# Kernel optimization log

Measured on AMD Instinct MI355X. Metric: run time of the kernel, lower is better.

## Reference

```python
import jax, jax.numpy as jnp
import numpy as np
import math

DIM = 1024
NUM_HEADS = 16
HEAD_DIM = DIM // NUM_HEADS


def build_rope_matrix(dim, seq_len):
    # (seq_len, dim): concat of cos(freqs) and sin(freqs), each (seq_len, dim//2)
    position = jnp.arange(seq_len, dtype=jnp.float32)[:, None]
    dim_pair = jnp.arange(0, dim, 2, dtype=jnp.float32)[None, :]
    theta = 10000.0 ** (-dim_pair / dim)
    freqs = position * theta  # (seq_len, dim//2)
    return jnp.concatenate([jnp.cos(freqs), jnp.sin(freqs)], axis=-1)


def apply_rope(x, rope):
    # x: (..., N, d), rope: (N, d). Faithful to the torch code's strided slicing.
    x1, x2 = x[..., ::2], x[..., 1::2]
    cos = rope[..., ::2]
    sin = rope[..., 1::2]
    return jnp.concatenate([x1 * cos - x2 * sin, x1 * sin + x2 * cos], axis=-1)


def setup_inputs() -> dict:
    key = jax.random.key(0)
    ks = jax.random.split(key, 9)
    B, N = 2, 2048
    x = jax.random.normal(ks[0], (B, N, DIM), dtype=jnp.float32)
    # Xavier-uniform-ish linear weights (dim, dim), zero-mean biases
    bound = math.sqrt(6.0 / (DIM + DIM))
    def w(k):
        return jax.random.uniform(k, (DIM, DIM), jnp.float32, -bound, bound)
    def b(k):
        return jax.random.uniform(k, (DIM,), jnp.float32, -1.0 / math.sqrt(DIM), 1.0 / math.sqrt(DIM))
    return {
        "x": x,
        "Wq": w(ks[1]), "bq": b(ks[2]),
        "Wk": w(ks[3]), "bk": b(ks[4]),
        "Wv": w(ks[5]), "bv": b(ks[6]),
        "Wo": w(ks[7]), "bo": b(ks[8]),
    }


def reference(x, Wq, bq, Wk, bk, Wv, bv, Wo, bo):
    B, N, _ = x.shape
    H, hd = NUM_HEADS, HEAD_DIM
    rope = build_rope_matrix(hd, N)  # (N, hd)

    def proj(W, bias):
        y = x @ W.T + bias               # (B, N, dim)
        return y.reshape(B, N, H, hd).transpose(0, 2, 1, 3)  # (B, H, N, hd)

    q = apply_rope(proj(Wq, bq), rope)
    k = apply_rope(proj(Wk, bk), rope)
    v = apply_rope(proj(Wv, bv), rope)

    scores = jnp.einsum("bhqd,bhkd->bhqk", q, k) / math.sqrt(hd)
    probs = jax.nn.softmax(scores, axis=-1)
    out = jnp.einsum("bhqk,bhkd->bhqd", probs, v)  # (B, H, N, hd)

    out = apply_rope(out, -rope)  # inverse RoPE (as defined: negate rope)
    out = out.transpose(0, 2, 1, 3).reshape(B, N, DIM)
    return out @ Wo.T + bo
```

## Files before the change

### kernel.cpp

```cpp
#include <hip/hip_runtime.h>
#include <hip/hip_bf16.h>
#include <math.h>

#define NHEADS 16
#define HDIM   64
#define BATCH  2
#define SEQLEN 2048
#define DIMSZ  1024

typedef _Float16 f16x8 __attribute__((ext_vector_type(8)));
typedef _Float16 f16x4 __attribute__((ext_vector_type(4)));
typedef float    f32x4 __attribute__((ext_vector_type(4)));
typedef unsigned short u16x8 __attribute__((ext_vector_type(8)));
typedef unsigned int   u32x4 __attribute__((ext_vector_type(4)));

__device__ __forceinline__ float rope_theta(int c) {
    int i = c & 31;
    return (float)pow(10000.0, -(double)i / 32.0);
}
__device__ __forceinline__ unsigned short f16u(float f) {
    _Float16 h = (_Float16)f;
    return *reinterpret_cast<unsigned short*>(&h);
}
__device__ __forceinline__ void async_copy16(const void* gsrc, void* lds) {
    __builtin_amdgcn_global_load_lds(
        (const __attribute__((address_space(1))) unsigned int*)gsrc,
        (__attribute__((address_space(3))) unsigned int*)lds, 16, 0, 0);
}

__global__ __launch_bounds__(256) void prep_kernel(
    const float* __restrict__ x, const float* __restrict__ Wq,
    const float* __restrict__ Wk, const float* __restrict__ Wv,
    const float* __restrict__ Wo, const float* __restrict__ bq,
    const float* __restrict__ bk, const float* __restrict__ bv,
    unsigned short* __restrict__ x16, unsigned short* __restrict__ Wqkv16,
    unsigned short* __restrict__ Wo16, float* __restrict__ biasqkv,
    float* __restrict__ ropeC, float* __restrict__ ropeS)
{
    const int NV = (4194304 + 4 * 1048576) / 8;
    int gid = blockIdx.x * 256 + threadIdx.x;
    for (int i = gid; i < NV; i += gridDim.x * 256) {
        long e = (long)i * 8;
        const float* src; unsigned short* dst; long off;
        if (e < 4194304)      { src = x;  dst = x16;              off = e; }
        else if (e < 5242880) { src = Wq; dst = Wqkv16;           off = e - 4194304; }
        else if (e < 6291456) { src = Wk; dst = Wqkv16 + 1048576; off = e - 5242880; }
        else if (e < 7340032) { src = Wv; dst = Wqkv16 + 2097152; off = e - 6291456; }
        else                  { src = Wo; dst = Wo16;             off = e - 7340032; }
        float4 v0 = *reinterpret_cast<const float4*>(src + off);
        float4 v1 = *reinterpret_cast<const float4*>(src + off + 4);
        u16x8 o;
        o[0] = f16u(v0.x); o[1] = f16u(v0.y); o[2] = f16u(v0.z); o[3] = f16u(v0.w);
        o[4] = f16u(v1.x); o[5] = f16u(v1.y); o[6] = f16u(v1.z); o[7] = f16u(v1.w);
        *reinterpret_cast<u16x8*>(dst + off) = o;
    }
    if (gid < 65536) {
        int npos = gid >> 5, j = gid & 31;
        float f = (float)npos * rope_theta(j);
        ropeC[gid] = cosf(f);
        ropeS[gid] = sinf(f);
    }
    if (gid < 3072) {
        biasqkv[gid] = gid < 1024 ? bq[gid] : (gid < 2048 ? bk[gid - 1024] : bv[gid - 2048]);
    }
}

__global__ __launch_bounds__(512, 4) void qkv_gemm_kernel(
    const unsigned short* __restrict__ A, const unsigned short* __restrict__ B,
    const float* __restrict__ bias, const float* __restrict__ ropeC,
    const float* __restrict__ ropeS, unsigned short* __restrict__ QKV)
{
    __shared__ __align__(16) unsigned char smem[65536];
    const int tid = threadIdx.x;
    const int w = tid >> 6, l = tid & 63;
    const int g = l >> 4, lx = l & 15;
    const int wr = w >> 2, wc = w & 3;
    const int row0 = blockIdx.y * 128;
    const int col0 = blockIdx.x * 128;
    const unsigned short* Ab = A + (size_t)row0 * DIMSZ;
    const unsigned short* Bb = B + (size_t)col0 * DIMSZ;

    const int sr = tid >> 3;
    const int sc = tid & 7;
    const int ssw = sc ^ (sr & 7);
    const size_t sAoff0 = (size_t)sr * DIMSZ + ssw * 8;
    const size_t sAoff1 = (size_t)(64 + sr) * DIMSZ + ssw * 8;

    f32x4 acc[4][2] = {};
    async_copy16(Ab + sAoff0, smem + tid * 16);
    async_copy16(Ab + sAoff1, smem + 8192 + tid * 16);
    async_copy16(Bb + sAoff0, smem + 16384 + tid * 16);
    async_copy16(Bb + sAoff1, smem + 16384 + 8192 + tid * 16);
    __syncthreads();

    int buf = 0;
    for (int k0 = 0; k0 < DIMSZ; k0 += 64) {
        if (k0 + 64 < DIMSZ) {
            const int nb = (buf ^ 1) * 32768;
            async_copy16(Ab + sAoff0 + k0 + 64, smem + nb + tid * 16);
            async_copy16(Ab + sAoff1 + k0 + 64, smem + nb + 8192 + tid * 16);
            async_copy16(Bb + sAoff0 + k0 + 64, smem + nb + 16384 + tid * 16);
            async_copy16(Bb + sAoff1 + k0 + 64, smem + nb + 16384 + 8192 + tid * 16);
        }
        const int ab = buf * 32768, bb2 = ab + 16384;
        #pragma unroll
        for (int ks = 0; ks < 2; ++ks) {
            f16x8 af[4], bf[2];
            #pragma unroll
            for (int m = 0; m < 4; ++m) {
                int r = wr * 64 + m * 16 + lx;
                af[m] = *reinterpret_cast<const f16x8*>(
                    &smem[ab + r * 128 + ((ks * 64 + g * 16) ^ ((r & 7) << 4))]);
            }
            #pragma unroll
            for (int n = 0; n < 2; ++n) {
                int r = wc * 32 + n * 16 + lx;
                bf[n] = *reinterpret_cast<const f16x8*>(
                    &smem[bb2 + r * 128 + ((ks * 64 + g * 16) ^ ((r & 7) << 4))]);
            }
            #pragma unroll
            for (int m = 0; m < 4; ++m)
                #pragma unroll
                for (int n = 0; n < 2; ++n)
                    acc[m][n] = __builtin_amdgcn_mfma_f32_16x16x32_f16(af[m], bf[n], acc[m][n], 0, 0, 0);
        }
        __syncthreads();
        buf ^= 1;
    }

    const int proj = col0 >> 10;
    const int cin128 = (col0 & 1023);
    float bsv[2];
    #pragma unroll
    for (int n = 0; n < 2; ++n) bsv[n] = bias[col0 + wc * 32 + n * 16 + lx];

    if (proj == 2) {
        _Float16* T = (_Float16*)smem;
        #pragma unroll
        for (int m = 0; m < 4; ++m) {
            int rl0 = wr * 64 + m * 16 + g * 4;
            #pragma unroll
            for (int r2 = 0; r2 < 4; ++r2) {
                int rlocal = rl0 + r2;
                int npos = (row0 + rlocal) & (SEQLEN - 1);
                const float* rcp = ropeC + npos * 32;
                const float* rsp = ropeS + npos * 32;
                #pragma unroll
                for (int n = 0; n < 2; ++n) {
                    float v = acc[m][n][r2] + bsv[n];
                    float o = __shfl_xor(v, 1);
                    int dcol = wc * 32 + n * 16 + lx;
                    int c = dcol & 63;
                    const float* tab = (c < 32) ? rcp : rsp;
                    float Rd = tab[c & 31];
                    float Rp = tab[(c & 31) ^ 1];
                    float y; int outc;
                    if (c & 1) { y = o * Rd + v * Rp; outc = (c >> 1) + 32; }
                    else       { y = v * Rd - o * Rp; outc = c >> 1; }
                    T[((dcol >> 6) * 64 + outc) * 136 + rlocal] = (_Float16)y;
                }
            }
        }
        __syncthreads();
        int b = row0 >> 11, npos0 = row0 & (SEQLEN - 1);
        int hd0 = cin128 >> 6;
        int trow = tid >> 2;
        int cbase = (tid & 3) * 32;
        int head = hd0 + (trow >> 6);
        int outd = trow & 63;
        unsigned short* vdst = QKV + 8388608 +
            (((size_t)b * NHEADS + head) * HDIM + outd) * SEQLEN + npos0 + cbase;
        #pragma unroll
        for (int i2 = 0; i2 < 4; ++i2) {
            f16x8 val = *reinterpret_cast<const f16x8*>(&T[trow * 136 + cbase + i2 * 8]);
            *reinterpret_cast<f16x8*>(vdst + i2 * 8) = val;
        }
    } else {
        #pragma unroll
        for (int m = 0; m < 4; ++m) {
            int rbase = row0 + wr * 64 + m * 16 + g * 4;
            #pragma unroll
            for (int r2 = 0; r2 < 4; ++r2) {
                int rglob = rbase + r2;
                int b = rglob >> 11, npos = rglob & (SEQLEN - 1);
                const float* rcp = ropeC + npos * 32;
                const float* rsp = ropeS + npos * 32;
                #pragma unroll
                for (int n = 0; n < 2; ++n) {
                    float v = acc[m][n][r2] + bsv[n];
                    float o = __shfl_xor(v, 1);
                    int hd = (cin128 + wc * 32 + n * 16) >> 6;
                    int c = ((wc * 32 + n * 16) & 63) + lx;
                    const float* tab = (c < 32) ? rcp : rsp;
                    float Rd = tab[c & 31];
                    float Rp = tab[(c & 31) ^ 1];
                    float y; int outc;
                    if (c & 1) { y = o * Rd + v * Rp; outc = (c >> 1) + 32; }
                    else       { y = v * Rd - o * Rp; outc = c >> 1; }
                    unsigned short* Orow = QKV +
                        ((((size_t)proj * BATCH + b) * NHEADS + hd) * SEQLEN + npos) * HDIM;
                    Orow[outc] = f16u(y);
                }
            }
        }
    }
}

__global__ __launch_bounds__(512, 8) void attn_mfma_kernel(
    const unsigned short* __restrict__ QKV, const float* __restrict__ ropeC,
    const float* __restrict__ ropeS, unsigned short* __restrict__ Y)
{
    __shared__ __align__(16) unsigned char smem[32768];
    const int tid = threadIdx.x;
    const int w   = tid >> 6;
    const int l   = tid & 63;
    const int g   = l >> 4;
    const int lx  = l & 15;
    const int qg  = w & 3;
    const int kh  = w >> 2;
    const int fb  = blockIdx.x;
    const int xcd = fb & 7, jj = fb >> 3;
    const int bh  = xcd * 4 + (jj & 3);
    const int b   = bh >> 4;
    const int h   = bh & 15;
    const int q0  = (jj >> 2) * 64;

    const unsigned short* Qb  = QKV + (size_t)bh * SEQLEN * HDIM;
    const unsigned short* Kb  = QKV + 4194304 + (size_t)bh * SEQLEN * HDIM;
    const unsigned short* Vtb = QKV + 8388608 + (size_t)bh * SEQLEN * HDIM;

    f16x8 qf[2];
    {
        const unsigned short* src = Qb + (size_t)(q0 + qg * 16 + lx) * HDIM + g * 8;
        qf[0] = *reinterpret_cast<const f16x8*>(src);
        qf[1] = *reinterpret_cast<const f16x8*>(src + 32);
    }
    f16x8 ones8;
    #pragma unroll
    for (int i = 0; i < 8; ++i) ones8[i] = (_Float16)1.0f;

    const float K2 = 0.18033688011112043f;
    f32x4 oacc[4] = {};
    f32x4 lsum = {};
    float mrow = -1e30f;

    const int srow = tid >> 3;
    const int c8   = tid & 7;
    const int sch  = c8 ^ (srow & 7);
    const int sdst = tid * 16;
    const int kperm = (srow & 32) + (((srow >> 2) & 3) << 3) + (((srow >> 4) & 1) << 2) + (srow & 3);

    async_copy16(Kb  + (size_t)kperm * HDIM + sch * 8, smem + sdst);
    async_copy16(Vtb + (size_t)srow * SEQLEN + sch * 8, smem + 8192 + sdst);
    __syncthreads();

    int buf = 0;
    for (int kt = 0; kt < SEQLEN / 64; ++kt) {
        if (kt + 1 < SEQLEN / 64) {
            const int k0n = (kt + 1) * 64;
            const int nb = (buf ^ 1) * 16384;
            async_copy16(Kb  + (size_t)(k0n + kperm) * HDIM + sch * 8,
                         smem + nb + sdst);
            async_copy16(Vtb + (size_t)srow * SEQLEN + k0n + sch * 8,
                         smem + nb + 8192 + sdst);
        }
        const int kb = buf * 16384;
        const int vb = kb + 8192;

        f32x4 sacc[2] = {};
        __builtin_amdgcn_s_setprio(1);
        #pragma unroll
        for (int c = 0; c < 2; ++c) {
            int row = kh * 32 + c * 16 + lx;
            int rowb = kb + row * 128, sw = (row & 7) << 4;
            f16x8 k0f = *reinterpret_cast<const f16x8*>(&smem[rowb + ((g * 16) ^ sw)]);
            f16x8 k1f = *reinterpret_cast<const f16x8*>(&smem[rowb + ((64 + g * 16) ^ sw)]);
            sacc[c] = __builtin_amdgcn_mfma_f32_16x16x32_f16(k0f, qf[0], sacc[c], 0, 0, 0);
            sacc[c] = __builtin_amdgcn_mfma_f32_16x16x32_f16(k1f, qf[1], sacc[c], 0, 0, 0);
        }
        __builtin_amdgcn_s_setprio(0);

        float lmax = sacc[0][0];
        #pragma unroll
        for (int c = 0; c < 2; ++c)
            #pragma unroll
            for (int r = 0; r < 4; ++r) lmax = fmaxf(lmax, sacc[c][r]);
        bool ok = (lmax <= mrow + 64.f);
        if (!__all((int)ok)) {
            float m2 = fmaxf(lmax, __shfl_xor(lmax, 16));
            m2 = fmaxf(m2, __shfl_xor(m2, 32));
            float mnew = fmaxf(mrow, m2);
            float sc = exp2f((mrow - mnew) * K2);
            mrow = mnew;
            #pragma unroll
            for (int r = 0; r < 4; ++r) lsum[r] *= sc;
            #pragma unroll
            for (int c = 0; c < 4; ++c)
                #pragma unroll
                for (int r = 0; r < 4; ++r) oacc[c][r] *= sc;
        }
        float mk = -mrow * K2;
        #pragma unroll
        for (int c = 0; c < 2; ++c)
            #pragma unroll
            for (int r = 0; r < 4; ++r)
                sacc[c][r] = exp2f(fmaf(sacc[c][r], K2, mk));

        u32x4 pw;
        pw[0] = __builtin_bit_cast(unsigned, __builtin_amdgcn_cvt_pkrtz(sacc[0][0], sacc[0][1]));
        pw[1] = __builtin_bit_cast(unsigned, __builtin_amdgcn_cvt_pkrtz(sacc[0][2], sacc[0][3]));
        pw[2] = __builtin_bit_cast(unsigned, __builtin_amdgcn_cvt_pkrtz(sacc[1][0], sacc[1][1]));
        pw[3] = __builtin_bit_cast(unsigned, __builtin_amdgcn_cvt_pkrtz(sacc[1][2], sacc[1][3]));
        f16x8 pfrag = __builtin_bit_cast(f16x8, pw);

        __builtin_amdgcn_s_setprio(1);
        lsum = __builtin_amdgcn_mfma_f32_16x16x32_f16(ones8, pfrag, lsum, 0, 0, 0);
        #pragma unroll
        for (int c2 = 0; c2 < 4; ++c2) {
            int d = c2 * 16 + lx;
            f16x8 vf8 = *reinterpret_cast<const f16x8*>(
                &smem[vb + d * 128 + ((kh * 64 + g * 16) ^ ((d & 7) << 4))]);
            oacc[c2] = __builtin_amdgcn_mfma_f32_16x16x32_f16(vf8, pfrag, oacc[c2], 0, 0, 0);
        }
        __builtin_amdgcn_s_setprio(0);

        __syncthreads();
        buf ^= 1;
    }

    float* Of = (float*)smem + qg * 1120;
    if (kh == 1) {
        #pragma unroll
        for (int c2 = 0; c2 < 4; ++c2)
            *reinterpret_cast<f32x4*>(&Of[lx * 68 + c2 * 16 + g * 4]) = oacc[c2];
        if (g == 0) {
            Of[1088 + lx] = mrow;
            Of[1104 + lx] = lsum[0];
        }
    }
    __syncthreads();
    if (kh == 0) {
        float m_hi = Of[1088 + lx];
        float l_hi = Of[1104 + lx];
        float M = fmaxf(mrow, m_hi);
        float a  = exp2f((mrow - M) * K2);
        float bb = exp2f((m_hi - M) * K2);
        float inv = 1.0f / (a * lsum[0] + bb * l_hi);
        const int q = q0 + qg * 16 + lx;
        unsigned short* drow = Y + ((size_t)b * SEQLEN + q) * DIMSZ + h * HDIM;
        #pragma unroll
        for (int c2 = 0; c2 < 4; ++c2) {
            f32x4 ohi = *reinterpret_cast<const f32x4*>(&Of[lx * 68 + c2 * 16 + g * 4]);
            const float* tab = ((c2 < 2) ? ropeC : ropeS) + (size_t)q * 32;
            unsigned short lo16[2], hi16[2];
            #pragma unroll
            for (int rp = 0; rp < 2; ++rp) {
                int d = c2 * 16 + g * 4 + 2 * rp;
                float v0 = (a * oacc[c2][2 * rp]     + bb * ohi[2 * rp])     * inv;
                float v1 = (a * oacc[c2][2 * rp + 1] + bb * ohi[2 * rp + 1]) * inv;
                float Rd = tab[d & 31], Rn = tab[(d & 31) + 1];
                lo16[rp] = f16u(-(v0 * Rd - v1 * Rn));
                hi16[rp] = f16u(-(v0 * Rn + v1 * Rd));
            }
            int p = c2 * 8 + g * 2;
            *reinterpret_cast<unsigned*>(&drow[p])      = (unsigned)lo16[0] | ((unsigned)lo16[1] << 16);
            *reinterpret_cast<unsigned*>(&drow[p + 32]) = (unsigned)hi16[0] | ((unsigned)hi16[1] << 16);
        }
    }
}

__global__ __launch_bounds__(512, 4) void out_gemm_kernel(
    const unsigned short* __restrict__ A, const unsigned short* __restrict__ B,
    const float* __restrict__ bias, float* __restrict__ Out)
{
    __shared__ __align__(16) unsigned char smem[65536];
    const int tid = threadIdx.x;
    const int w = tid >> 6, l = tid & 63;
    const int g = l >> 4, lx = l & 15;
    const int wr = w >> 2, wc = w & 3;
    const int row0 = blockIdx.y * 128;
    const int col0 = blockIdx.x * 128;
    const unsigned short* Ab = A + (size_t)row0 * DIMSZ;
    const unsigned short* Bb = B + (size_t)col0 * DIMSZ;

    const int sr = tid >> 3;
    const int sc = tid & 7;
    const int ssw = sc ^ (sr & 7);
    const size_t sAoff0 = (size_t)sr * DIMSZ + ssw * 8;
    const size_t sAoff1 = (size_t)(64 + sr) * DIMSZ + ssw * 8;

    f32x4 acc[4][2] = {};
    async_copy16(Ab + sAoff0, smem + tid * 16);
    async_copy16(Ab + sAoff1, smem + 8192 + tid * 16);
    async_copy16(Bb + sAoff0, smem + 16384 + tid * 16);
    async_copy16(Bb + sAoff1, smem + 16384 + 8192 + tid * 16);
    __syncthreads();

    int buf = 0;
    for (int k0 = 0; k0 < DIMSZ; k0 += 64) {
        if (k0 + 64 < DIMSZ) {
            const int nb = (buf ^ 1) * 32768;
            async_copy16(Ab + sAoff0 + k0 + 64, smem + nb + tid * 16);
            async_copy16(Ab + sAoff1 + k0 + 64, smem + nb + 8192 + tid * 16);
            async_copy16(Bb + sAoff0 + k0 + 64, smem + nb + 16384 + tid * 16);
            async_copy16(Bb + sAoff1 + k0 + 64, smem + nb + 16384 + 8192 + tid * 16);
        }
        const int ab = buf * 32768, bb2 = ab + 16384;
        #pragma unroll
        for (int ks = 0; ks < 2; ++ks) {
            f16x8 af[4], bf[2];
            #pragma unroll
            for (int m = 0; m < 4; ++m) {
                int r = wr * 64 + m * 16 + lx;
                af[m] = *reinterpret_cast<const f16x8*>(
                    &smem[ab + r * 128 + ((ks * 64 + g * 16) ^ ((r & 7) << 4))]);
            }
            #pragma unroll
            for (int n = 0; n < 2; ++n) {
                int r = wc * 32 + n * 16 + lx;
                bf[n] = *reinterpret_cast<const f16x8*>(
                    &smem[bb2 + r * 128 + ((ks * 64 + g * 16) ^ ((r & 7) << 4))]);
            }
            #pragma unroll
            for (int m = 0; m < 4; ++m)
                #pragma unroll
                for (int n = 0; n < 2; ++n)
                    acc[m][n] = __builtin_amdgcn_mfma_f32_16x16x32_f16(af[m], bf[n], acc[m][n], 0, 0, 0);
        }
        __syncthreads();
        buf ^= 1;
    }

    const int cb0 = col0 + wc * 32;
    float bsv[2];
    #pragma unroll
    for (int n = 0; n < 2; ++n) bsv[n] = bias[cb0 + n * 16 + lx];
    #pragma unroll
    for (int m = 0; m < 4; ++m) {
        int rbase = row0 + wr * 64 + m * 16 + g * 4;
        #pragma unroll
        for (int r2 = 0; r2 < 4; ++r2) {
            float* orow = Out + (size_t)(rbase + r2) * DIMSZ + cb0;
            #pragma unroll
            for (int n = 0; n < 2; ++n)
                orow[n * 16 + lx] = acc[m][n][r2] + bsv[n];
        }
    }
}

extern "C" void kernel_launch(void* const* d_in, const int* in_sizes, int n_in,
                              void* d_out, int out_size, void* d_ws, size_t ws_size,
                              hipStream_t stream) {
    const float* x  = (const float*)d_in[0];
    const float* Wq = (const float*)d_in[1];
    const float* bq = (const float*)d_in[2];
    const float* Wk = (const float*)d_in[3];
    const float* bk = (const float*)d_in[4];
    const float* Wv = (const float*)d_in[5];
    const float* bv = (const float*)d_in[6];
    const float* Wo = (const float*)d_in[7];
    const float* bo = (const float*)d_in[8];
    float* out = (float*)d_out;

    char* ws = (char*)d_ws;
    unsigned short* x16    = (unsigned short*)(ws);
    unsigned short* Wqkv16 = (unsigned short*)(ws + 8388608);
    unsigned short* Wo16   = (unsigned short*)(ws + 14680064);
    float* biasqkv         = (float*)(ws + 16777216);
    float* ropeC           = (float*)(ws + 16793600);
    float* ropeS           = (float*)(ws + 17055744);
    unsigned short* QKVw   = (unsigned short*)(ws + 17825792);
    unsigned short* Yw     = (unsigned short*)(ws + 42991616);

    prep_kernel<<<dim3(2048), dim3(256), 0, stream>>>(x, Wq, Wk, Wv, Wo, bq, bk, bv,
                                                x16, Wqkv16, Wo16, biasqkv, ropeC, ropeS);
    qkv_gemm_kernel<<<dim3(24, 32), dim3(512), 0, stream>>>(x16, Wqkv16, biasqkv, ropeC, ropeS, QKVw);
    attn_mfma_kernel<<<dim3(1024), dim3(512), 0, stream>>>(QKVw, ropeC, ropeS, Yw);
    out_gemm_kernel<<<dim3(8, 32), dim3(512), 0, stream>>>(Yw, Wo16, bo, out);
}
```

Before: 135.3 us.

## Process two query tiles per warp in attention to reuse K/V fragments

Each attention block now covers 128 queries instead of 64, with every warp handling two 16-row query tiles that share the same K and V fragments read from LDS. This halves the block count and the global K/V traffic per query, and amortises LDS reads across twice the MFMA work. LDS addressing is precomputed and toggled by XOR, and shared memory grows to hold the larger merge scratch. In exchange, register pressure rises (launch bounds drop to 4 waves per SIMD) and only 512 blocks are launched, which may leave the GPU less occupied.

```diff
diff --git a/kernel.cpp b/kernel.cpp
--- a/kernel.cpp
+++ b/kernel.cpp
@@ -9,7 +9,6 @@
 #define DIMSZ  1024
 
 typedef _Float16 f16x8 __attribute__((ext_vector_type(8)));
-typedef _Float16 f16x4 __attribute__((ext_vector_type(4)));
 typedef float    f32x4 __attribute__((ext_vector_type(4)));
 typedef unsigned short u16x8 __attribute__((ext_vector_type(8)));
 typedef unsigned int   u32x4 __attribute__((ext_vector_type(4)));
@@ -206,11 +205,11 @@
     }
 }
 
-__global__ __launch_bounds__(512, 8) void attn_mfma_kernel(
+__global__ __launch_bounds__(512, 4) void attn_mfma_kernel(
     const unsigned short* __restrict__ QKV, const float* __restrict__ ropeC,
     const float* __restrict__ ropeS, unsigned short* __restrict__ Y)
 {
-    __shared__ __align__(16) unsigned char smem[32768];
+    __shared__ __align__(16) unsigned char smem[36864];
     const int tid = threadIdx.x;
     const int w   = tid >> 6;
     const int l   = tid & 63;
@@ -223,148 +222,156 @@
     const int bh  = xcd * 4 + (jj & 3);
     const int b   = bh >> 4;
     const int h   = bh & 15;
-    const int q0  = (jj >> 2) * 64;
+    const int q0  = (jj >> 2) * 128;
 
     const unsigned short* Qb  = QKV + (size_t)bh * SEQLEN * HDIM;
     const unsigned short* Kb  = QKV + 4194304 + (size_t)bh * SEQLEN * HDIM;
     const unsigned short* Vtb = QKV + 8388608 + (size_t)bh * SEQLEN * HDIM;
 
-    f16x8 qf[2];
-    {
-        const unsigned short* src = Qb + (size_t)(q0 + qg * 16 + lx) * HDIM + g * 8;
-        qf[0] = *reinterpret_cast<const f16x8*>(src);
-        qf[1] = *reinterpret_cast<const f16x8*>(src + 32);
+    f16x8 qf[2][2];
+    #pragma unroll
+    for (int qt = 0; qt < 2; ++qt) {
+        const unsigned short* src = Qb + (size_t)(q0 + qg * 32 + qt * 16 + lx) * HDIM + g * 8;
+        qf[qt][0] = *reinterpret_cast<const f16x8*>(src);
+        qf[qt][1] = *reinterpret_cast<const f16x8*>(src + 32);
     }
     f16x8 ones8;
     #pragma unroll
     for (int i = 0; i < 8; ++i) ones8[i] = (_Float16)1.0f;
 
     const float K2 = 0.18033688011112043f;
-    f32x4 oacc[4] = {};
-    f32x4 lsum = {};
-    float mrow = -1e30f;
+    f32x4 oacc[2][4] = {};
+    f32x4 lsum[2] = {};
+    float mrow[2] = {-1e30f, -1e30f};
 
     const int srow = tid >> 3;
     const int c8   = tid & 7;
     const int sch  = c8 ^ (srow & 7);
     const int sdst = tid * 16;
     const int kperm = (srow & 32) + (((srow >> 2) & 3) << 3) + (((srow >> 4) & 1) << 2) + (srow & 3);
-
-    async_copy16(Kb  + (size_t)kperm * HDIM + sch * 8, smem + sdst);
-    async_copy16(Vtb + (size_t)srow * SEQLEN + sch * 8, smem + 8192 + sdst);
+    const unsigned short* Kp = Kb + (size_t)kperm * HDIM + sch * 8;
+    const unsigned short* Vp = Vtb + (size_t)srow * SEQLEN + sch * 8;
+
+    async_copy16(Kp, smem + sdst);
+    async_copy16(Vp, smem + 8192 + sdst);
+    Kp += 64 * HDIM; Vp += 64;
     __syncthreads();
 
-    int buf = 0;
+    const int sw = (lx & 7) << 4;
+    unsigned kb0 = (kh * 32 + lx) * 128 + ((g * 16) ^ sw);
+    unsigned kb1 = (kh * 32 + lx) * 128 + ((64 + g * 16) ^ sw);
+    unsigned vb0 = 8192 + lx * 128 + ((kh * 64 + g * 16) ^ sw);
+    unsigned nst = 16384 + sdst;
+
     for (int kt = 0; kt < SEQLEN / 64; ++kt) {
         if (kt + 1 < SEQLEN / 64) {
-            const int k0n = (kt + 1) * 64;
-            const int nb = (buf ^ 1) * 16384;
-            async_copy16(Kb  + (size_t)(k0n + kperm) * HDIM + sch * 8,
-                         smem + nb + sdst);
-            async_copy16(Vtb + (size_t)srow * SEQLEN + k0n + sch * 8,
-                         smem + nb + 8192 + sdst);
-        }
-        const int kb = buf * 16384;
-        const int vb = kb + 8192;
-
-        f32x4 sacc[2] = {};
+            async_copy16(Kp, smem + nst);
+            async_copy16(Vp, smem + 8192 + nst);
+            Kp += 64 * HDIM; Vp += 64;
+        }
+
+        f16x8 kf00 = *reinterpret_cast<const f16x8*>(&smem[kb0]);
+        f16x8 kf01 = *reinterpret_cast<const f16x8*>(&smem[kb1]);
+        f16x8 kf10 = *reinterpret_cast<const f16x8*>(&smem[kb0 + 2048]);
+        f16x8 kf11 = *reinterpret_cast<const f16x8*>(&smem[kb1 + 2048]);
+
+        f16x8 pfrag[2];
+        #pragma unroll
+        for (int qt = 0; qt < 2; ++qt) {
+            f32x4 s0 = {}, s1 = {};
+            __builtin_amdgcn_s_setprio(1);
+            s0 = __builtin_amdgcn_mfma_f32_16x16x32_f16(kf00, qf[qt][0], s0, 0, 0, 0);
+            s0 = __builtin_amdgcn_mfma_f32_16x16x32_f16(kf01, qf[qt][1], s0, 0, 0, 0);
+            s1 = __builtin_amdgcn_mfma_f32_16x16x32_f16(kf10, qf[qt][0], s1, 0, 0, 0);
+            s1 = __builtin_amdgcn_mfma_f32_16x16x32_f16(kf11, qf[qt][1], s1, 0, 0, 0);
+            __builtin_amdgcn_s_setprio(0);
+
+            float lmax = fmaxf(fmaxf(fmaxf(s0[0], s0[1]), fmaxf(s0[2], s0[3])),
+                               fmaxf(fmaxf(s1[0], s1[1]), fmaxf(s1[2], s1[3])));
+            bool ok = (lmax <= mrow[qt] + 64.f);
+            if (!__all((int)ok)) {
+                float m2 = fmaxf(lmax, __shfl_xor(lmax, 16));
+                m2 = fmaxf(m2, __shfl_xor(m2, 32));
+                float mnew = fmaxf(mrow[qt], m2);
+                float sc = exp2f((mrow[qt] - mnew) * K2);
+                mrow[qt] = mnew;
+                lsum[qt] *= sc;
+                #pragma unroll
+                for (int c2 = 0; c2 < 4; ++c2) oacc[qt][c2] *= sc;
+            }
+            float mk = -mrow[qt] * K2;
+            #pragma unroll
+            for (int r = 0; r < 4; ++r) {
+                s0[r] = exp2f(fmaf(s0[r], K2, mk));
+                s1[r] = exp2f(fmaf(s1[r], K2, mk));
+            }
+            u32x4 pw;
+            pw[0] = __builtin_bit_cast(unsigned, __builtin_amdgcn_cvt_pkrtz(s0[0], s0[1]));
+            pw[1] = __builtin_bit_cast(unsigned, __builtin_amdgcn_cvt_pkrtz(s0[2], s0[3]));
+            pw[2] = __builtin_bit_cast(unsigned, __builtin_amdgcn_cvt_pkrtz(s1[0], s1[1]));
+            pw[3] = __builtin_bit_cast(unsigned, __builtin_amdgcn_cvt_pkrtz(s1[2], s1[3]));
+            pfrag[qt] = __builtin_bit_cast(f16x8, pw);
+        }
+
         __builtin_amdgcn_s_setprio(1);
-        #pragma unroll
-        for (int c = 0; c < 2; ++c) {
-            int row = kh * 32 + c * 16 + lx;
-            int rowb = kb + row * 128, sw = (row & 7) << 4;
-            f16x8 k0f = *reinterpret_cast<const f16x8*>(&smem[rowb + ((g * 16) ^ sw)]);
-            f16x8 k1f = *reinterpret_cast<const f16x8*>(&smem[rowb + ((64 + g * 16) ^ sw)]);
-            sacc[c] = __builtin_amdgcn_mfma_f32_16x16x32_f16(k0f, qf[0], sacc[c], 0, 0, 0);
-            sacc[c] = __builtin_amdgcn_mfma_f32_16x16x32_f16(k1f, qf[1], sacc[c], 0, 0, 0);
+        lsum[0] = __builtin_amdgcn_mfma_f32_16x16x32_f16(ones8, pfrag[0], lsum[0], 0, 0, 0);
+        lsum[1] = __builtin_amdgcn_mfma_f32_16x16x32_f16(ones8, pfrag[1], lsum[1], 0, 0, 0);
+        #pragma unroll
+        for (int c2 = 0; c2 < 4; ++c2) {
+            f16x8 vf = *reinterpret_cast<const f16x8*>(&smem[vb0 + c2 * 2048]);
+            oacc[0][c2] = __builtin_amdgcn_mfma_f32_16x16x32_f16(vf, pfrag[0], oacc[0][c2], 0, 0, 0);
+            oacc[1][c2] = __builtin_amdgcn_mfma_f32_16x16x32_f16(vf, pfrag[1], oacc[1][c2], 0, 0, 0);
         }
         __builtin_amdgcn_s_setprio(0);
 
-        float lmax = sacc[0][0];
-        #pragma unroll
-        for (int c = 0; c < 2; ++c)
-            #pragma unroll
-            for (int r = 0; r < 4; ++r) lmax = fmaxf(lmax, sacc[c][r]);
-        bool ok = (lmax <= mrow + 64.f);
-        if (!__all((int)ok)) {
-            float m2 = fmaxf(lmax, __shfl_xor(lmax, 16));
-            m2 = fmaxf(m2, __shfl_xor(m2, 32));
-            float mnew = fmaxf(mrow, m2);
-            float sc = exp2f((mrow - mnew) * K2);
-            mrow = mnew;
-            #pragma unroll
-            for (int r = 0; r < 4; ++r) lsum[r] *= sc;
-            #pragma unroll
-            for (int c = 0; c < 4; ++c)
-                #pragma unroll
-                for (int r = 0; r < 4; ++r) oacc[c][r] *= sc;
-        }
-        float mk = -mrow * K2;
-        #pragma unroll
-        for (int c = 0; c < 2; ++c)
-            #pragma unroll
-            for (int r = 0; r < 4; ++r)
-                sacc[c][r] = exp2f(fmaf(sacc[c][r], K2, mk));
-
-        u32x4 pw;
-        pw[0] = __builtin_bit_cast(unsigned, __builtin_amdgcn_cvt_pkrtz(sacc[0][0], sacc[0][1]));
-        pw[1] = __builtin_bit_cast(unsigned, __builtin_amdgcn_cvt_pkrtz(sacc[0][2], sacc[0][3]));
-        pw[2] = __builtin_bit_cast(unsigned, __builtin_amdgcn_cvt_pkrtz(sacc[1][0], sacc[1][1]));
-        pw[3] = __builtin_bit_cast(unsigned, __builtin_amdgcn_cvt_pkrtz(sacc[1][2], sacc[1][3]));
-        f16x8 pfrag = __builtin_bit_cast(f16x8, pw);
-
-        __builtin_amdgcn_s_setprio(1);
-        lsum = __builtin_amdgcn_mfma_f32_16x16x32_f16(ones8, pfrag, lsum, 0, 0, 0);
-        #pragma unroll
-        for (int c2 = 0; c2 < 4; ++c2) {
-            int d = c2 * 16 + lx;
-            f16x8 vf8 = *reinterpret_cast<const f16x8*>(
-                &smem[vb + d * 128 + ((kh * 64 + g * 16) ^ ((d & 7) << 4))]);
-            oacc[c2] = __builtin_amdgcn_mfma_f32_16x16x32_f16(vf8, pfrag, oacc[c2], 0, 0, 0);
-        }
-        __builtin_amdgcn_s_setprio(0);
-
         __syncthreads();
-        buf ^= 1;
-    }
-
-    float* Of = (float*)smem + qg * 1120;
+        kb0 ^= 16384; kb1 ^= 16384; vb0 ^= 16384; nst ^= 16384;
+    }
+
     if (kh == 1) {
         #pragma unroll
-        for (int c2 = 0; c2 < 4; ++c2)
-            *reinterpret_cast<f32x4*>(&Of[lx * 68 + c2 * 16 + g * 4]) = oacc[c2];
-        if (g == 0) {
-            Of[1088 + lx] = mrow;
-            Of[1104 + lx] = lsum[0];
+        for (int qt = 0; qt < 2; ++qt) {
+            float* Of = (float*)smem + (qg * 2 + qt) * 1120;
+            #pragma unroll
+            for (int c2 = 0; c2 < 4; ++c2)
+                *reinterpret_cast<f32x4*>(&Of[lx * 68 + c2 * 16 + g * 4]) = oacc[qt][c2];
+            if (g == 0) {
+                Of[1088 + lx] = mrow[qt];
+                Of[1104 + lx] = lsum[qt][0];
+            }
         }
     }
     __syncthreads();
     if (kh == 0) {
-        float m_hi = Of[1088 + lx];
-        float l_hi = Of[1104 + lx];
-        float M = fmaxf(mrow, m_hi);
-        float a  = exp2f((mrow - M) * K2);
-        float bb = exp2f((m_hi - M) * K2);
-        float inv = 1.0f / (a * lsum[0] + bb * l_hi);
-        const int q = q0 + qg * 16 + lx;
-        unsigned short* drow = Y + ((size_t)b * SEQLEN + q) * DIMSZ + h * HDIM;
-        #pragma unroll
-        for (int c2 = 0; c2 < 4; ++c2) {
-            f32x4 ohi = *reinterpret_cast<const f32x4*>(&Of[lx * 68 + c2 * 16 + g * 4]);
-            const float* tab = ((c2 < 2) ? ropeC : ropeS) + (size_t)q * 32;
-            unsigned short lo16[2], hi16[2];
-            #pragma unroll
-            for (int rp = 0; rp < 2; ++rp) {
-                int d = c2 * 16 + g * 4 + 2 * rp;
-                float v0 = (a * oacc[c2][2 * rp]     + bb * ohi[2 * rp])     * inv;
-                float v1 = (a * oacc[c2][2 * rp + 1] + bb * ohi[2 * rp + 1]) * inv;
-                float Rd = tab[d & 31], Rn = tab[(d & 31) + 1];
-                lo16[rp] = f16u(-(v0 * Rd - v1 * Rn));
-                hi16[rp] = f16u(-(v0 * Rn + v1 * Rd));
-            }
-            int p = c2 * 8 + g * 2;
-            *reinterpret_cast<unsigned*>(&drow[p])      = (unsigned)lo16[0] | ((unsigned)lo16[1] << 16);
-            *reinterpret_cast<unsigned*>(&drow[p + 32]) = (unsigned)hi16[0] | ((unsigned)hi16[1] << 16);
+        #pragma unroll
+        for (int qt = 0; qt < 2; ++qt) {
+            float* Of = (float*)smem + (qg * 2 + qt) * 1120;
+            float m_hi = Of[1088 + lx];
+            float l_hi = Of[1104 + lx];
+            float M = fmaxf(mrow[qt], m_hi);
+            float a  = exp2f((mrow[qt] - M) * K2);
+            float bb = exp2f((m_hi - M) * K2);
+            float inv = 1.0f / (a * lsum[qt][0] + bb * l_hi);
+            const int q = q0 + qg * 32 + qt * 16 + lx;
+            unsigned short* drow = Y + ((size_t)b * SEQLEN + q) * DIMSZ + h * HDIM;
+            #pragma unroll
+            for (int c2 = 0; c2 < 4; ++c2) {
+                f32x4 ohi = *reinterpret_cast<const f32x4*>(&Of[lx * 68 + c2 * 16 + g * 4]);
+                const float* tab = ((c2 < 2) ? ropeC : ropeS) + (size_t)q * 32;
+                unsigned short lo16[2], hi16[2];
+                #pragma unroll
+                for (int rp = 0; rp < 2; ++rp) {
+                    int d = c2 * 16 + g * 4 + 2 * rp;
+                    float v0 = (a * oacc[qt][c2][2 * rp]     + bb * ohi[2 * rp])     * inv;
+                    float v1 = (a * oacc[qt][c2][2 * rp + 1] + bb * ohi[2 * rp + 1]) * inv;
+                    float Rd = tab[d & 31], Rn = tab[(d & 31) + 1];
+                    lo16[rp] = f16u(-(v0 * Rd - v1 * Rn));
+                    hi16[rp] = f16u(-(v0 * Rn + v1 * Rd));
+                }
+                int p = c2 * 8 + g * 2;
+                *reinterpret_cast<unsigned*>(&drow[p])      = (unsigned)lo16[0] | ((unsigned)lo16[1] << 16);
+                *reinterpret_cast<unsigned*>(&drow[p + 32]) = (unsigned)hi16[0] | ((unsigned)hi16[1] << 16);
+            }
         }
     }
 }
@@ -475,6 +482,6 @@
     prep_kernel<<<dim3(2048), dim3(256), 0, stream>>>(x, Wq, Wk, Wv, Wo, bq, bk, bv,
                                                 x16, Wqkv16, Wo16, biasqkv, ropeC, ropeS);
     qkv_gemm_kernel<<<dim3(24, 32), dim3(512), 0, stream>>>(x16, Wqkv16, biasqkv, ropeC, ropeS, QKVw);
-    attn_mfma_kernel<<<dim3(1024), dim3(512), 0, stream>>>(QKVw, ropeC, ropeS, Yw);
+    attn_mfma_kernel<<<dim3(512), dim3(512), 0, stream>>>(QKVw, ropeC, ropeS, Yw);
     out_gemm_kernel<<<dim3(8, 32), dim3(512), 0, stream>>>(Yw, Wo16, bo, out);
 }
```

Measured after the change: 136.0 us. Within noise of the previous version (+0.6%).
